# Kernel optimization log

Measured on AMD Instinct MI355X. Metric: run time of the kernel, lower is better.

## Reference

```python
import jax, jax.numpy as jnp
import numpy as np

D = 1024
H = 16
HD = D // H
MLP = 4 * D


def _lin(key, fin, fout):
    k1, k2 = jax.random.split(key)
    lim = 1.0 / np.sqrt(fin)
    W = jax.random.uniform(k1, (fin, fout), minval=-lim, maxval=lim, dtype=jnp.float32)
    b = jax.random.uniform(k2, (fout,), minval=-lim, maxval=lim, dtype=jnp.float32)
    return W, b


def setup_inputs() -> dict:
    key = jax.random.key(0)
    ks = jax.random.split(key, 10)
    x = jax.random.normal(ks[0], (4, 2048, D), dtype=jnp.float32)
    time_emb = jax.random.normal(ks[1], (4, D), dtype=jnp.float32)
    Wqkv, bqkv = _lin(ks[2], D, 3 * D)
    Wproj, bproj = _lin(ks[3], D, D)
    W1, b1 = _lin(ks[4], D, MLP)
    W2, b2 = _lin(ks[5], MLP, D)
    Wt, bt = _lin(ks[6], D, 6 * D)
    g1 = jnp.ones((D,), jnp.float32); be1 = jnp.zeros((D,), jnp.float32)
    g2 = jnp.ones((D,), jnp.float32); be2 = jnp.zeros((D,), jnp.float32)
    return {"x": x, "time_emb": time_emb, "Wqkv": Wqkv, "bqkv": bqkv,
            "Wproj": Wproj, "bproj": bproj, "W1": W1, "b1": b1, "W2": W2, "b2": b2,
            "Wt": Wt, "bt": bt, "g1": g1, "be1": be1, "g2": g2, "be2": be2}


def layernorm(x, g, b, eps=1e-5):
    mu = jnp.mean(x, axis=-1, keepdims=True)
    var = jnp.var(x, axis=-1, keepdims=True)
    return (x - mu) * jax.lax.rsqrt(var + eps) * g + b


def attention(h, Wqkv, bqkv, Wproj, bproj):
    B, L, _ = h.shape
    qkv = (h @ Wqkv + bqkv).reshape(B, L, 3, H, HD)
    q, k, v = jnp.moveaxis(qkv, 2, 0)  # each [B,L,H,HD]
    scale = HD ** -0.5
    attn = jnp.einsum('blhd,bmhd->bhlm', q, k) * scale
    attn = jax.nn.softmax(attn, axis=-1)
    out = jnp.einsum('bhlm,bmhd->blhd', attn, v).reshape(B, L, D)
    return out @ Wproj + bproj


def reference(x, time_emb, Wqkv, bqkv, Wproj, bproj, W1, b1, W2, b2, Wt, bt, g1, be1, g2, be2):
    tp = (jax.nn.silu(time_emb) @ Wt + bt)[:, None, :]  # [B,1,6D]
    shift_msa, scale_msa, gate_msa, shift_mlp, scale_mlp, gate_mlp = jnp.split(tp, 6, axis=-1)
    h = layernorm(x, g1, be1)
    h = h * (1.0 + scale_msa) + shift_msa
    h = attention(h, Wqkv, bqkv, Wproj, bproj)
    x = x + gate_msa * h
    h = layernorm(x, g2, be2)
    h = h * (1.0 + scale_mlp) + shift_mlp
    h = jax.nn.gelu(h @ W1 + b1, approximate=False) @ W2 + b2
    x = x + gate_mlp * h
    return x
```

## Files before the change

kernel.cpp:

```cpp
#include <hip/hip_runtime.h>
#include <hip/hip_bf16.h>
#include <math.h>


typedef __attribute__((ext_vector_type(8))) __bf16 bf16x8;
typedef __attribute__((ext_vector_type(4))) float f32x4;

union FragU { uint4 u; bf16x8 b; };

#define AS1(p) ((const __attribute__((address_space(1))) void*)(p))
#define AS3(p) ((__attribute__((address_space(3))) void*)(p))

__device__ __forceinline__ float bflo(uint u) {
    union { uint i; float f; } v; v.i = u << 16; return v.f;
}
__device__ __forceinline__ ushort f2bf(float f) {
    union { float f; uint i; } v; v.f = f;
    uint r = (v.i + 0x7fffu + ((v.i >> 16) & 1u)) >> 16;
    return (ushort)r;
}
__device__ __forceinline__ uint pkbf(float a, float b) {
    return __builtin_amdgcn_perm(__float_as_uint(b), __float_as_uint(a), 0x07060302u);
}
__device__ __forceinline__ void stval(ushort* p, float v) { *p = f2bf(v); }
__device__ __forceinline__ void stval(float* p, float v) { *p = v; }

__device__ __forceinline__ float gelu_f(float x) {
    float y = 0.7978845608f * (x + 0.044715f * x * x * x);
    float e = exp2f(y * 2.88539008178f);
    float t = 1.f - 2.f / (1.f + e);
    return 0.5f * x * (1.f + t);
}

__global__ __launch_bounds__(256) void transpose_f2b(const float* __restrict__ in,
                                                     ushort* __restrict__ out,
                                                     int R, int C) {
    __shared__ ushort t[32][33];
    int c0 = blockIdx.x * 32, r0 = blockIdx.y * 32;
    int tx = threadIdx.x, ty = threadIdx.y;
#pragma unroll
    for (int i = 0; i < 32; i += 8)
        t[ty + i][tx] = f2bf(in[(size_t)(r0 + ty + i) * C + c0 + tx]);
    __syncthreads();
#pragma unroll
    for (int i = 0; i < 32; i += 8)
        out[(size_t)(c0 + ty + i) * R + r0 + tx] = t[tx][ty + i];
}

__global__ __launch_bounds__(256) void transpose_v(const ushort* __restrict__ qkv,
                                                   ushort* __restrict__ vT) {
    int bh = blockIdx.x >> 5, lt = blockIdx.x & 31;
    int b = bh >> 4, h = bh & 15;
    int d = threadIdx.x & 63, lg = threadIdx.x >> 6;
    const ushort* src = qkv + (size_t)b * 2048 * 3072 + 2048 + h * 64 + d;
#pragma unroll
    for (int g = 0; g < 2; g++) {
        int l0 = lt * 64 + lg * 16 + g * 8;
        ushort v[8];
#pragma unroll
        for (int i = 0; i < 8; i++) v[i] = src[(size_t)(l0 + i) * 3072];
        *(uint4*)&vT[((size_t)bh * 64 + d) * 2048 + l0] = *(uint4*)v;
    }
}

__global__ __launch_bounds__(256) void tp_gemm(const float* __restrict__ te,
                                               const ushort* __restrict__ WtT,
                                               const float* __restrict__ bt,
                                               float* __restrict__ tp) {
    int w = blockIdx.x * 4 + (threadIdx.x >> 6);
    int lane = threadIdx.x & 63;
    int b = w / 6144, n = w % 6144;
    const ushort* wr = WtT + (size_t)n * 1024;
    const float* tr = te + (size_t)b * 1024;
    float s = 0.f;
#pragma unroll
    for (int i = 0; i < 16; i++) {
        int k = lane + 64 * i;
        float t = tr[k];
        float sil = t / (1.f + __expf(-t));
        s += sil * bflo((uint)wr[k]);
    }
#pragma unroll
    for (int x = 32; x; x >>= 1) s += __shfl_xor(s, x);
    if (lane == 0) tp[(size_t)b * 6144 + n] = s + bt[n];
}

__global__ __launch_bounds__(256) void ln_mod(const float* __restrict__ x,
                                              const float* __restrict__ tpb,
                                              const float* __restrict__ g,
                                              const float* __restrict__ be,
                                              ushort* __restrict__ out,
                                              int shift_off, int scale_off) {
    __shared__ float2 sred[4];
    int row = blockIdx.x;
    int b = row >> 11;
    int tid = threadIdx.x;
    float4 f = *(const float4*)&x[(size_t)row * 1024 + tid * 4];
    float v[4] = {f.x, f.y, f.z, f.w};
    float s = v[0] + v[1] + v[2] + v[3];
    float s2 = v[0] * v[0] + v[1] * v[1] + v[2] * v[2] + v[3] * v[3];
#pragma unroll
    for (int m = 32; m; m >>= 1) { s += __shfl_xor(s, m); s2 += __shfl_xor(s2, m); }
    if ((tid & 63) == 0) sred[tid >> 6] = make_float2(s, s2);
    __syncthreads();
    s = sred[0].x + sred[1].x + sred[2].x + sred[3].x;
    s2 = sred[0].y + sred[1].y + sred[2].y + sred[3].y;
    float mu = s * (1.f / 1024.f);
    float var = s2 * (1.f / 1024.f) - mu * mu;
    float rs = rsqrtf(var + 1e-5f);
    const float* tprow = tpb + (size_t)b * 6144;
    ushort o4[4];
#pragma unroll
    for (int t = 0; t < 4; t++) {
        int c = tid * 4 + t;
        float y = (v[t] - mu) * rs * g[c] + be[c];
        y = y * (1.f + tprow[scale_off + c]) + tprow[shift_off + c];
        o4[t] = f2bf(y);
    }
    *(uint2*)&out[(size_t)row * 1024 + tid * 4] = *(uint2*)o4;
}

template <int EPI, typename OT>
__global__ __launch_bounds__(256) void gemm_bt(const ushort* __restrict__ A,
                                               const ushort* __restrict__ BT,
                                               const float* __restrict__ bias,
                                               OT* __restrict__ C,
                                               int M, int N, int K,
                                               const float* __restrict__ res,
                                               const float* __restrict__ tpb,
                                               int goff, int sccols) {
    __shared__ __align__(16) ushort As[2][128 * 32];
    __shared__ __align__(16) ushort Bs[2][128 * 32];
    int m0 = blockIdx.y * 128, n0 = blockIdx.x * 128;
    int tid = threadIdx.x;
    int wid = tid >> 6, lane = tid & 63;
    int wy = wid >> 1, wx = wid & 1;
    int r16 = lane & 15;
    int q8 = (lane >> 4) << 3;

    f32x4 acc[4][4];
#pragma unroll
    for (int i = 0; i < 4; i++)
#pragma unroll
        for (int j = 0; j < 4; j++) acc[i][j] = (f32x4){0.f, 0.f, 0.f, 0.f};

    int sr = tid >> 2;
    int sc = (tid & 3) << 3;
    const ushort* Abase = A + (size_t)(m0 + sr) * K + sc;
    const ushort* Bbase = BT + (size_t)(n0 + sr) * K + sc;

    for (int k0 = 0; k0 < K; k0 += 64) {
#pragma unroll
        for (int c = 0; c < 2; c++) {
            ushort* AsW = As[c] + wid * 512;
            ushort* BsW = Bs[c] + wid * 512;
            int kk = k0 + 32 * c;
            __builtin_amdgcn_global_load_lds(AS1(Abase + kk), AS3(AsW), 16, 0, 0);
            __builtin_amdgcn_global_load_lds(AS1(Abase + (size_t)64 * K + kk), AS3(AsW + 2048), 16, 0, 0);
            __builtin_amdgcn_global_load_lds(AS1(Bbase + kk), AS3(BsW), 16, 0, 0);
            __builtin_amdgcn_global_load_lds(AS1(Bbase + (size_t)64 * K + kk), AS3(BsW + 2048), 16, 0, 0);
        }
        __syncthreads();
#pragma unroll
        for (int c = 0; c < 2; c++) {
            FragU fa[4], fb[4];
#pragma unroll
            for (int i = 0; i < 4; i++)
                fa[i].u = *(const uint4*)&As[c][(wy * 64 + i * 16 + r16) * 32 + q8];
#pragma unroll
            for (int j = 0; j < 4; j++)
                fb[j].u = *(const uint4*)&Bs[c][(wx * 64 + j * 16 + r16) * 32 + q8];
#pragma unroll
            for (int i = 0; i < 4; i++)
#pragma unroll
                for (int j = 0; j < 4; j++)
                    acc[i][j] = __builtin_amdgcn_mfma_f32_16x16x32_bf16(fa[i].b, fb[j].b, acc[i][j], 0, 0, 0);
        }
        __syncthreads();
    }

    int q4 = (lane >> 4) << 2;
#pragma unroll
    for (int i = 0; i < 4; i++) {
#pragma unroll
        for (int j = 0; j < 4; j++) {
            int col = n0 + wx * 64 + j * 16 + r16;
            float bv = bias[col];
#pragma unroll
            for (int t = 0; t < 4; t++) {
                int row = m0 + wy * 64 + i * 16 + q4 + t;
                float v = acc[i][j][t] + bv;
                if constexpr (EPI == 0) {
                    if (col < sccols) v *= 0.18033688011f;
                }
                if constexpr (EPI == 1) {
                    v = gelu_f(v);
                }
                if constexpr (EPI == 2) {
                    float rv = res[(size_t)row * N + col];
                    float gate = tpb[(size_t)(row >> 11) * 6144 + goff + col];
                    v = rv + gate * v;
                }
                stval(&C[(size_t)row * N + col], v);
            }
        }
    }
}

__global__ __launch_bounds__(512, 4) void attn_mfma(const ushort* __restrict__ qkv,
                                                    const ushort* __restrict__ vT,
                                                    ushort* __restrict__ out) {
    __shared__ __align__(16) ushort Ks[2][64 * 72];
    __shared__ __align__(16) ushort Vs[2][64 * 72];
    __shared__ __align__(16) ushort Ps[256 * 72];

    int tid = threadIdx.x;
    int wid = tid >> 6, lane = tid & 63;
    int r16 = lane & 15, quad = lane >> 4;
    int q8 = quad << 3, q4 = quad << 2;

    int bh = blockIdx.x >> 3;
    int qt = blockIdx.x & 7;
    int b = bh >> 4, h = bh & 15;
    const ushort* qkbase = qkv + (size_t)b * 2048 * 3072 + h * 64;

    int kr = tid >> 3;
    int kc = (tid & 7) << 3;
    const ushort* kptr = qkbase + 1024 + (size_t)kr * 3072 + kc;
    const ushort* vptr = vT + (size_t)bh * 131072 + (size_t)kr * 2048 + kc;

    uint4 ka = *(const uint4*)kptr;
    uint4 va = *(const uint4*)vptr;

    {
        int r = tid >> 1;
        int c = (tid & 1) << 5;
        const ushort* qp = qkbase + (size_t)(qt * 256 + r) * 3072 + c;
        *(uint4*)&Ps[r * 72 + c]      = *(const uint4*)qp;
        *(uint4*)&Ps[r * 72 + c + 8]  = *(const uint4*)(qp + 8);
        *(uint4*)&Ps[r * 72 + c + 16] = *(const uint4*)(qp + 16);
        *(uint4*)&Ps[r * 72 + c + 24] = *(const uint4*)(qp + 24);
    }
    __syncthreads();
    FragU qa[2][2];
#pragma unroll
    for (int qm = 0; qm < 2; qm++)
#pragma unroll
        for (int ks = 0; ks < 2; ks++)
            qa[qm][ks].u = *(const uint4*)&Ps[(wid * 32 + qm * 16 + r16) * 72 + ks * 32 + q8];

    *(uint4*)&Ks[0][kr * 72 + kc] = ka;
    *(uint4*)&Vs[0][kr * 72 + kc] = va;
    ka = *(const uint4*)(kptr + (size_t)64 * 3072);
    va = *(const uint4*)(vptr + 64);
    __syncthreads();

    float l4[2][4] = {{0.f, 0.f, 0.f, 0.f}, {0.f, 0.f, 0.f, 0.f}};
    f32x4 o[2][4];
#pragma unroll
    for (int qm = 0; qm < 2; qm++)
#pragma unroll
        for (int dn = 0; dn < 4; dn++) o[qm][dn] = (f32x4){0.f, 0.f, 0.f, 0.f};

    for (int kt = 0; kt < 32; kt++) {
        int cur = kt & 1;
        const ushort* ksb = Ks[cur];
        const ushort* vsb = Vs[cur];

        if (kt < 31) {
            *(uint4*)&Ks[cur ^ 1][kr * 72 + kc] = ka;
            *(uint4*)&Vs[cur ^ 1][kr * 72 + kc] = va;
        }

        FragU kb[2][4];
#pragma unroll
        for (int ks = 0; ks < 2; ks++)
#pragma unroll
            for (int n = 0; n < 4; n++)
                kb[ks][n].u = *(const uint4*)&ksb[(n * 16 + r16) * 72 + ks * 32 + q8];
#pragma unroll
        for (int qm = 0; qm < 2; qm++) {
            f32x4 s[4];
#pragma unroll
            for (int n = 0; n < 4; n++) s[n] = (f32x4){0.f, 0.f, 0.f, 0.f};
#pragma unroll
            for (int ks = 0; ks < 2; ks++)
#pragma unroll
                for (int n = 0; n < 4; n++)
                    s[n] = __builtin_amdgcn_mfma_f32_16x16x32_bf16(kb[ks][n].b, qa[qm][ks].b, s[n], 0, 0, 0);
#pragma unroll
            for (int n = 0; n < 4; n++) {
                float p0 = exp2f(s[n][0]);
                float p1 = exp2f(s[n][1]);
                float p2 = exp2f(s[n][2]);
                float p3 = exp2f(s[n][3]);
                l4[qm][0] += p0; l4[qm][1] += p1; l4[qm][2] += p2; l4[qm][3] += p3;
                uint2 w2 = make_uint2(pkbf(p0, p1), pkbf(p2, p3));
                *(uint2*)&Ps[(wid * 32 + qm * 16 + r16) * 72 + n * 16 + q4] = w2;
            }
        }

        if (kt < 30) {
            ka = *(const uint4*)(kptr + (size_t)(kt + 2) * 64 * 3072);
            va = *(const uint4*)(vptr + (kt + 2) * 64);
        }

#pragma unroll
        for (int ks = 0; ks < 2; ks++) {
            FragU vb[4], pa0, pa1;
#pragma unroll
            for (int dn = 0; dn < 4; dn++)
                vb[dn].u = *(const uint4*)&vsb[(dn * 16 + r16) * 72 + ks * 32 + q8];
            pa0.u = *(const uint4*)&Ps[(wid * 32 + r16) * 72 + ks * 32 + q8];
            pa1.u = *(const uint4*)&Ps[(wid * 32 + 16 + r16) * 72 + ks * 32 + q8];
#pragma unroll
            for (int dn = 0; dn < 4; dn++) {
                o[0][dn] = __builtin_amdgcn_mfma_f32_16x16x32_bf16(vb[dn].b, pa0.b, o[0][dn], 0, 0, 0);
                o[1][dn] = __builtin_amdgcn_mfma_f32_16x16x32_bf16(vb[dn].b, pa1.b, o[1][dn], 0, 0, 0);
            }
        }

        __syncthreads();
    }

#pragma unroll
    for (int qm = 0; qm < 2; qm++) {
        float l_ = (l4[qm][0] + l4[qm][1]) + (l4[qm][2] + l4[qm][3]);
        l_ += __shfl_xor(l_, 16);
        l_ += __shfl_xor(l_, 32);
        float inv = 1.f / l_;
        int row = qt * 256 + wid * 32 + qm * 16 + r16;
        ushort* orow = out + (size_t)(b * 2048 + row) * 1024 + h * 64;
#pragma unroll
        for (int dn = 0; dn < 4; dn++) {
            uint2 w2 = make_uint2(pkbf(o[qm][dn][0] * inv, o[qm][dn][1] * inv),
                                  pkbf(o[qm][dn][2] * inv, o[qm][dn][3] * inv));
            *(uint2*)&orow[dn * 16 + q4] = w2;
        }
    }
}

extern "C" void kernel_launch(void* const* d_in, const int* in_sizes, int n_in,
                              void* d_out, int out_size, void* d_ws, size_t ws_size,
                              hipStream_t stream) {
    const float* x    = (const float*)d_in[0];
    const float* te   = (const float*)d_in[1];
    const float* Wqkv = (const float*)d_in[2];
    const float* bqkv = (const float*)d_in[3];
    const float* Wproj= (const float*)d_in[4];
    const float* bproj= (const float*)d_in[5];
    const float* W1   = (const float*)d_in[6];
    const float* b1   = (const float*)d_in[7];
    const float* W2   = (const float*)d_in[8];
    const float* b2   = (const float*)d_in[9];
    const float* Wt   = (const float*)d_in[10];
    const float* bt   = (const float*)d_in[11];
    const float* g1   = (const float*)d_in[12];
    const float* be1  = (const float*)d_in[13];
    const float* g2   = (const float*)d_in[14];
    const float* be2  = (const float*)d_in[15];

    char* ws = (char*)d_ws;
    ushort* WqkvT  = (ushort*)(ws + 0);
    ushort* WprojT = (ushort*)(ws + 6291456);
    ushort* W1T    = (ushort*)(ws + 8388608);
    ushort* W2T    = (ushort*)(ws + 16777216);
    ushort* WtT    = (ushort*)(ws + 25165824);
    float*  tpb    = (float*)(ws + 37748736);
    ushort* hbuf   = (ushort*)(ws + 37847040);
    ushort* vTb    = (ushort*)(ws + 37847040);
    ushort* qkvb   = (ushort*)(ws + 54624256);
    ushort* midb   = (ushort*)(ws + 54624256);
    ushort* attnb  = (ushort*)(ws + 121733120);
    float*  x1b    = (float*)(ws + 138510336);

    dim3 tb(32, 8);
    hipLaunchKernelGGL(transpose_f2b, dim3(3072 / 32, 1024 / 32), tb, 0, stream, Wqkv, WqkvT, 1024, 3072);
    hipLaunchKernelGGL(transpose_f2b, dim3(1024 / 32, 1024 / 32), tb, 0, stream, Wproj, WprojT, 1024, 1024);
    hipLaunchKernelGGL(transpose_f2b, dim3(4096 / 32, 1024 / 32), tb, 0, stream, W1, W1T, 1024, 4096);
    hipLaunchKernelGGL(transpose_f2b, dim3(1024 / 32, 4096 / 32), tb, 0, stream, W2, W2T, 4096, 1024);
    hipLaunchKernelGGL(transpose_f2b, dim3(6144 / 32, 1024 / 32), tb, 0, stream, Wt, WtT, 1024, 6144);

    hipLaunchKernelGGL(tp_gemm, dim3(6144), dim3(256), 0, stream, te, WtT, bt, tpb);

    hipLaunchKernelGGL(ln_mod, dim3(8192), dim3(256), 0, stream, x, tpb, g1, be1, hbuf, 0, 1024);

    hipLaunchKernelGGL((gemm_bt<0, ushort>), dim3(3072 / 128, 8192 / 128), dim3(256), 0, stream,
                       hbuf, WqkvT, bqkv, qkvb, 8192, 3072, 1024, (const float*)nullptr, (const float*)nullptr, 0, 1024);

    hipLaunchKernelGGL(transpose_v, dim3(2048), dim3(256), 0, stream, qkvb, vTb);

    hipLaunchKernelGGL(attn_mfma, dim3(512), dim3(512), 0, stream, qkvb, vTb, attnb);

    hipLaunchKernelGGL((gemm_bt<2, float>), dim3(1024 / 128, 8192 / 128), dim3(256), 0, stream,
                       attnb, WprojT, bproj, x1b, 8192, 1024, 1024, x, tpb, 2048, 0);

    hipLaunchKernelGGL(ln_mod, dim3(8192), dim3(256), 0, stream, x1b, tpb, g2, be2, hbuf, 3072, 4096);

    hipLaunchKernelGGL((gemm_bt<1, ushort>), dim3(4096 / 128, 8192 / 128), dim3(256), 0, stream,
                       hbuf, W1T, b1, midb, 8192, 4096, 1024, (const float*)nullptr, (const float*)nullptr, 0, 0);

    hipLaunchKernelGGL((gemm_bt<2, float>), dim3(1024 / 128, 8192 / 128), dim3(256), 0, stream,
                       midb, W2T, b2, (float*)d_out, 8192, 1024, 4096, x1b, tpb, 5120, 0);
}
```

Measured before the change: 622.2 us.

## Add 256x256-tile 8-wave GEMM with interleaved LDS staging for QKV and MLP-up

Adds a new bf16 MFMA GEMM kernel using 256x256 block tiles, 512 threads (8 waves), double-buffered async global-to-LDS loads, and MFMA phases interleaved with barriers and priority hints. It replaces the 128x128 GEMM for the QKV projection and the first MLP linear, aiming for higher arithmetic intensity and better overlap of loads with compute. The larger tile uses 128 KB of LDS and many accumulator registers, which may limit occupancy, and it yields fewer blocks (384 and 512) relative to the CU count.

```diff
diff --git a/kernel.cpp b/kernel.cpp
--- a/kernel.cpp
+++ b/kernel.cpp
@@ -202,6 +202,133 @@
                     v = rv + gate * v;
                 }
                 stval(&C[(size_t)row * N + col], v);
+            }
+        }
+    }
+}
+
+template <int EPI>
+__global__ __launch_bounds__(512, 2) void gemm_8ph(const ushort* __restrict__ A,
+                                                   const ushort* __restrict__ BT,
+                                                   const float* __restrict__ bias,
+                                                   ushort* __restrict__ C,
+                                                   int M, int N, int K, int sccols) {
+    __shared__ __align__(16) ushort La[2][256 * 64];
+    __shared__ __align__(16) ushort Lb[2][256 * 64];
+    int tid = threadIdx.x;
+    int wid = tid >> 6, lane = tid & 63;
+    int wm = wid >> 2, wn = wid & 3;
+    int r16 = lane & 15;
+    int q8 = (lane >> 4) << 3, q4 = (lane >> 4) << 2;
+    int m0 = blockIdx.y * 256, n0 = blockIdx.x * 256;
+
+    int sr = tid >> 3;
+    int sc = (tid & 7) << 3;
+    const ushort* Ab = A + (size_t)(m0 + sr) * K + sc;
+    const ushort* Bb = BT + (size_t)(n0 + sr) * K + sc;
+
+    f32x4 acc[8][4];
+#pragma unroll
+    for (int i = 0; i < 8; i++)
+#pragma unroll
+        for (int j = 0; j < 4; j++) acc[i][j] = (f32x4){0.f, 0.f, 0.f, 0.f};
+
+    auto STAGE = [&](int t) {
+        int p = t & 1;
+        int kk = t << 6;
+#pragma unroll
+        for (int i = 0; i < 4; i++) {
+            __builtin_amdgcn_global_load_lds(AS1(Ab + (size_t)i * 64 * K + kk),
+                                             AS3(&La[p][i * 4096 + wid * 512]), 16, 0, 0);
+            __builtin_amdgcn_global_load_lds(AS1(Bb + (size_t)i * 64 * K + kk),
+                                             AS3(&Lb[p][i * 4096 + wid * 512]), 16, 0, 0);
+        }
+    };
+
+    int NT = K >> 6;
+    STAGE(0);
+    STAGE(1);
+    asm volatile("s_waitcnt vmcnt(8)" ::: "memory");
+    __builtin_amdgcn_sched_barrier(0);
+    __builtin_amdgcn_s_barrier();
+
+    for (int t = 0; t < NT; t++) {
+        int cur = t & 1;
+        const ushort* la = La[cur];
+        const ushort* lb = Lb[cur];
+        FragU fa[4][2], fb[4][2], fa2[4][2];
+#pragma unroll
+        for (int i = 0; i < 4; i++)
+#pragma unroll
+            for (int kk = 0; kk < 2; kk++)
+                fa[i][kk].u = *(const uint4*)&la[(wm * 128 + i * 16 + r16) * 64 + kk * 32 + q8];
+#pragma unroll
+        for (int j = 0; j < 4; j++)
+#pragma unroll
+            for (int kk = 0; kk < 2; kk++)
+                fb[j][kk].u = *(const uint4*)&lb[(wn * 64 + j * 16 + r16) * 64 + kk * 32 + q8];
+        __builtin_amdgcn_s_setprio(1);
+#pragma unroll
+        for (int i = 0; i < 4; i++)
+#pragma unroll
+            for (int j = 0; j < 4; j++)
+#pragma unroll
+                for (int kk = 0; kk < 2; kk++)
+                    acc[i][j] = __builtin_amdgcn_mfma_f32_16x16x32_bf16(fa[i][kk].b, fb[j][kk].b, acc[i][j], 0, 0, 0);
+        __builtin_amdgcn_s_setprio(0);
+#pragma unroll
+        for (int i = 0; i < 4; i++)
+#pragma unroll
+            for (int kk = 0; kk < 2; kk++)
+                fa2[i][kk].u = *(const uint4*)&la[(wm * 128 + 64 + i * 16 + r16) * 64 + kk * 32 + q8];
+        __builtin_amdgcn_s_setprio(1);
+#pragma unroll
+        for (int i = 0; i < 4; i++)
+#pragma unroll
+            for (int j = 0; j < 2; j++)
+#pragma unroll
+                for (int kk = 0; kk < 2; kk++)
+                    acc[4 + i][j] = __builtin_amdgcn_mfma_f32_16x16x32_bf16(fa2[i][kk].b, fb[j][kk].b, acc[4 + i][j], 0, 0, 0);
+        __builtin_amdgcn_s_setprio(0);
+        asm volatile("s_waitcnt lgkmcnt(0)" ::: "memory");
+        __builtin_amdgcn_sched_barrier(0);
+        __builtin_amdgcn_s_barrier();
+        if (t + 2 < NT) STAGE(t + 2);
+        __builtin_amdgcn_s_setprio(1);
+#pragma unroll
+        for (int i = 0; i < 4; i++)
+#pragma unroll
+            for (int j = 2; j < 4; j++)
+#pragma unroll
+                for (int kk = 0; kk < 2; kk++)
+                    acc[4 + i][j] = __builtin_amdgcn_mfma_f32_16x16x32_bf16(fa2[i][kk].b, fb[j][kk].b, acc[4 + i][j], 0, 0, 0);
+        __builtin_amdgcn_s_setprio(0);
+        if (t + 2 < NT) {
+            asm volatile("s_waitcnt vmcnt(8)" ::: "memory");
+        } else {
+            asm volatile("s_waitcnt vmcnt(0)" ::: "memory");
+        }
+        __builtin_amdgcn_sched_barrier(0);
+        __builtin_amdgcn_s_barrier();
+    }
+
+#pragma unroll
+    for (int i = 0; i < 8; i++) {
+        int rbase = m0 + wm * 128 + (i >> 2) * 64 + (i & 3) * 16 + q4;
+#pragma unroll
+        for (int j = 0; j < 4; j++) {
+            int col = n0 + wn * 64 + j * 16 + r16;
+            float bv = bias[col];
+#pragma unroll
+            for (int tt = 0; tt < 4; tt++) {
+                float v = acc[i][j][tt] + bv;
+                if constexpr (EPI == 0) {
+                    if (col < sccols) v *= 0.18033688011f;
+                }
+                if constexpr (EPI == 1) {
+                    v = gelu_f(v);
+                }
+                C[(size_t)(rbase + tt) * N + col] = f2bf(v);
             }
         }
     }
@@ -385,8 +512,8 @@
 
     hipLaunchKernelGGL(ln_mod, dim3(8192), dim3(256), 0, stream, x, tpb, g1, be1, hbuf, 0, 1024);
 
-    hipLaunchKernelGGL((gemm_bt<0, ushort>), dim3(3072 / 128, 8192 / 128), dim3(256), 0, stream,
-                       hbuf, WqkvT, bqkv, qkvb, 8192, 3072, 1024, (const float*)nullptr, (const float*)nullptr, 0, 1024);
+    hipLaunchKernelGGL((gemm_8ph<0>), dim3(3072 / 256, 8192 / 256), dim3(512), 0, stream,
+                       hbuf, WqkvT, bqkv, qkvb, 8192, 3072, 1024, 1024);
 
     hipLaunchKernelGGL(transpose_v, dim3(2048), dim3(256), 0, stream, qkvb, vTb);
 
@@ -397,8 +524,8 @@
 
     hipLaunchKernelGGL(ln_mod, dim3(8192), dim3(256), 0, stream, x1b, tpb, g2, be2, hbuf, 3072, 4096);
 
-    hipLaunchKernelGGL((gemm_bt<1, ushort>), dim3(4096 / 128, 8192 / 128), dim3(256), 0, stream,
-                       hbuf, W1T, b1, midb, 8192, 4096, 1024, (const float*)nullptr, (const float*)nullptr, 0, 0);
+    hipLaunchKernelGGL((gemm_8ph<1>), dim3(4096 / 256, 8192 / 256), dim3(512), 0, stream,
+                       hbuf, W1T, b1, midb, 8192, 4096, 1024, 0);
 
     hipLaunchKernelGGL((gemm_bt<2, float>), dim3(1024 / 128, 8192 / 128), dim3(256), 0, stream,
                        midb, W2T, b2, (float*)d_out, 8192, 1024, 4096, x1b, tpb, 5120, 0);
```

Result: no change. 632.1 us (+1.6%).
